# Kernel optimization log

Measured on AMD Instinct MI355X. Metric: run time of the kernel, lower is better.

The kernel has to match this reference:

```python
import jax, jax.numpy as jnp
import numpy as np

N_NODES = 50000
N_EDGES = 1600000
D = 128  # in_dim = hidden = out_dim = 128


def _gat_layer(x, W, b, aW, ab, src, dst, n_nodes):
    # fc: z = x @ W^T + b   (torch Linear convention, W:[out,in])
    z = x @ W.T + b                      # [N, d]
    d = z.shape[1]
    # attn_fc(concat(z_src, z_dst)) decomposed into per-node halves
    a_src = z @ aW[0, :d]                # [N]
    a_dst = z @ aW[0, d:]                # [N]
    e = jax.nn.leaky_relu(a_src[src] + a_dst[dst] + ab[0])  # [E], slope 0.01 (torch default)
    # segment softmax over incoming edges of each dst node
    m = jax.ops.segment_max(e, dst, num_segments=n_nodes)   # [N]
    ex = jnp.exp(e - m[dst])             # [E]
    s = jax.ops.segment_sum(ex, dst, num_segments=n_nodes)  # [N]
    alpha = ex / s[dst]                  # [E]
    # weighted scatter-sum of source features
    h = jax.ops.segment_sum(alpha[:, None] * z[src], dst, num_segments=n_nodes)  # [N, d]
    return h


def setup_inputs() -> dict:
    key = jax.random.key(0)
    ks = jax.random.split(key, 16)
    x = jax.random.normal(ks[0], (N_NODES, D), dtype=jnp.float32)
    src = jax.random.randint(ks[1], (N_EDGES,), 0, N_NODES, dtype=jnp.int32)
    dst = jax.random.randint(ks[2], (N_EDGES,), 0, N_NODES, dtype=jnp.int32)
    inp = {"x": x, "src": src, "dst": dst, "t": 0}
    # 3 GAT layers (128->128, 128->128, 128->128); xavier-ish scale
    for i in range(3):
        base = 3 + 4 * i
        inp[f"W{i}"] = jax.random.normal(ks[base], (D, D), dtype=jnp.float32) * (1.0 / np.sqrt(D))
        inp[f"b{i}"] = jnp.zeros((D,), dtype=jnp.float32)
        inp[f"aW{i}"] = jax.random.normal(ks[base + 1], (1, 2 * D), dtype=jnp.float32) * (1.0 / np.sqrt(2 * D))
        inp[f"ab{i}"] = jnp.zeros((1,), dtype=jnp.float32)
    return inp


def reference(x, src, dst, t, W0, b0, aW0, ab0, W1, b1, aW1, ab1, W2, b2, aW2, ab2):
    n = x.shape[0]
    h = _gat_layer(x, W0, b0, aW0, ab0, src, dst, n)
    h = jax.nn.relu(h)
    h = _gat_layer(h, W1, b1, aW1, ab1, src, dst, n)
    h = jax.nn.relu(h)
    h = _gat_layer(h, W2, b2, aW2, ab2, src, dst, n)
    return h
```

## Files before the change

### kernel.cpp

```cpp
#include <hip/hip_runtime.h>
#include <hip/hip_fp16.h>
#include <math.h>

#define DD 128
#define NBKT 391
#define P1CHUNK 4096
#define P2CAP 8192


__global__ __launch_bounds__(256) void fill_zero_i(int* p, int n) {
    int i = blockIdx.x * 256 + threadIdx.x;
    if (i < n) p[i] = 0;
}


__global__ __launch_bounds__(512) void p1hist_k(const int* __restrict__ dst, int* __restrict__ gcount, int E) {
    __shared__ int lh[NBKT];
    const int tid = threadIdx.x;
    for (int i = tid; i < NBKT; i += 512) lh[i] = 0;
    __syncthreads();
    const int blk0 = blockIdx.x * P1CHUNK;
    const int blkE = min(blk0 + P1CHUNK, E);
    int i0 = blk0 + tid * 8;
    if (i0 + 8 <= blkE) {
        int4 d0 = *reinterpret_cast<const int4*>(dst + i0);
        int4 d1 = *reinterpret_cast<const int4*>(dst + i0 + 4);
        atomicAdd(&lh[d0.x >> 7], 1); atomicAdd(&lh[d0.y >> 7], 1);
        atomicAdd(&lh[d0.z >> 7], 1); atomicAdd(&lh[d0.w >> 7], 1);
        atomicAdd(&lh[d1.x >> 7], 1); atomicAdd(&lh[d1.y >> 7], 1);
        atomicAdd(&lh[d1.z >> 7], 1); atomicAdd(&lh[d1.w >> 7], 1);
    } else {
        for (int j = 0; j < 8; ++j) {
            int i = i0 + j;
            if (i < blkE) atomicAdd(&lh[dst[i] >> 7], 1);
        }
    }
    __syncthreads();
    for (int i = tid; i < NBKT; i += 512)
        if (lh[i]) atomicAdd(&gcount[i], lh[i]);
}


__global__ __launch_bounds__(512) void p1scan_k(const int* __restrict__ gcount, int* __restrict__ bbase,
                                                int* __restrict__ bcur, int E) {
    __shared__ int tmp[512];
    int t = threadIdx.x;
    int v = (t < NBKT) ? gcount[t] : 0;
    tmp[t] = v;
    __syncthreads();
#pragma unroll
    for (int o = 1; o < 512; o <<= 1) {
        int add = (t >= o) ? tmp[t - o] : 0;
        __syncthreads();
        tmp[t] += add;
        __syncthreads();
    }
    if (t <= NBKT) {
        int ex = (t < NBKT) ? (tmp[t] - v) : E;
        bbase[t] = ex;
        if (t < NBKT) bcur[t] = ex;
    }
}


__global__ __launch_bounds__(512) void p1scatter_k(const int* __restrict__ src, const int* __restrict__ dst,
                                                   int* __restrict__ bcur, int2* __restrict__ bufA, int E) {
    __shared__ int lcnt[NBKT];
    __shared__ int lstart[512];
    __shared__ int blkb[NBKT];
    __shared__ int2 stage[P1CHUNK];
    const int tid = threadIdx.x;
    for (int i = tid; i < NBKT; i += 512) lcnt[i] = 0;
    __syncthreads();
    const int blk0 = blockIdx.x * P1CHUNK;
    const int blkE = min(blk0 + P1CHUNK, E);
    const int i0 = blk0 + tid * 8;

    int sv[8], dv[8], bn[8], rk[8], cntT = 0;
    if (i0 + 8 <= blkE) {
        int4 s0 = *reinterpret_cast<const int4*>(src + i0);
        int4 s1 = *reinterpret_cast<const int4*>(src + i0 + 4);
        int4 d0 = *reinterpret_cast<const int4*>(dst + i0);
        int4 d1 = *reinterpret_cast<const int4*>(dst + i0 + 4);
        sv[0] = s0.x; sv[1] = s0.y; sv[2] = s0.z; sv[3] = s0.w;
        sv[4] = s1.x; sv[5] = s1.y; sv[6] = s1.z; sv[7] = s1.w;
        dv[0] = d0.x; dv[1] = d0.y; dv[2] = d0.z; dv[3] = d0.w;
        dv[4] = d1.x; dv[5] = d1.y; dv[6] = d1.z; dv[7] = d1.w;
        cntT = 8;
    } else {
#pragma unroll
        for (int j = 0; j < 8; ++j) {
            int i = i0 + j;
            if (i < blkE) { sv[j] = src[i]; dv[j] = dst[i]; cntT = j + 1; }
        }
    }
#pragma unroll
    for (int j = 0; j < 8; ++j) {
        if (j < cntT) {
            bn[j] = dv[j] >> 7;
            rk[j] = atomicAdd(&lcnt[bn[j]], 1);
        }
    }
    __syncthreads();
    int v = (tid < NBKT) ? lcnt[tid] : 0;
    lstart[tid] = v;
    __syncthreads();
#pragma unroll
    for (int o = 1; o < 512; o <<= 1) {
        int add = (tid >= o) ? lstart[tid - o] : 0;
        __syncthreads();
        lstart[tid] += add;
        __syncthreads();
    }
    lstart[tid] -= v;
    __syncthreads();
    for (int i = tid; i < NBKT; i += 512)
        blkb[i] = lcnt[i] ? atomicAdd(&bcur[i], lcnt[i]) : 0;
#pragma unroll
    for (int j = 0; j < 8; ++j) {
        if (j < cntT) {
            int pos = lstart[bn[j]] + rk[j];
            stage[pos] = make_int2(sv[j], dv[j]);
        }
    }
    __syncthreads();
    const int cnt = blkE - blk0;
    for (int j = tid; j < cnt; j += 512) {
        int2 e = stage[j];
        int b = e.y >> 7;
        bufA[blkb[b] + (j - lstart[b])] = e;
    }
}


__global__ __launch_bounds__(512) void p2sort_k(const int2* __restrict__ bufA, const int* __restrict__ bbase,
                                                int* __restrict__ srcs, int* __restrict__ dstS) {
    __shared__ int h2[128];
    __shared__ int start2[128];
    __shared__ int cur2[128];
    __shared__ int ssrc[P2CAP];
    __shared__ int sdst[P2CAP];
    const int tid = threadIdx.x;
    const int b = blockIdx.x;
    const int base = bbase[b];
    const int cnt = bbase[b + 1] - base;
    for (int i = tid; i < 128; i += 512) h2[i] = 0;
    __syncthreads();
    for (int j = tid; j < cnt; j += 512)
        atomicAdd(&h2[bufA[base + j].y & 127], 1);
    __syncthreads();
    if (tid == 0) {
        int s = 0;
        for (int i = 0; i < 128; ++i) { start2[i] = s; cur2[i] = s; s += h2[i]; }
    }
    __syncthreads();
    for (int j = tid; j < cnt; j += 512) {
        int2 e = bufA[base + j];
        int p = atomicAdd(&cur2[e.y & 127], 1);
        ssrc[p] = e.x;
        sdst[p] = e.y;
    }
    __syncthreads();
    for (int j = tid; j < cnt; j += 512) {
        srcs[base + j] = ssrc[j];
        dstS[base + j] = sdst[j];
    }
}


__global__ __launch_bounds__(512) void off_k(const int* __restrict__ dstS, int* __restrict__ off, int N, int E) {
    int i = blockIdx.x * 512 + threadIdx.x;
    if (i >= E) return;
    int d = dstS[i];
    int p = (i == 0) ? -1 : dstS[i - 1];
    if (d != p)
        for (int n = p + 1; n <= d; ++n) off[n] = i;
    if (i == E - 1)
        for (int n = d + 1; n <= N; ++n) off[n] = E;
}


__global__ __launch_bounds__(256) void gemm_k(const float* __restrict__ X, const float* __restrict__ W,
                                              const float* __restrict__ B, const float* __restrict__ aW,
                                              __half* __restrict__ Zh, float* __restrict__ a_src,
                                              float* __restrict__ a_dst, int N) {
    __shared__ __align__(16) float xs[32][64];
    __shared__ __align__(16) float ws[32][128];
    const int tid = threadIdx.x;
    const int row0 = blockIdx.x * 64;
    const int cg = tid & 31;
    const int rg = tid >> 5;
    float acc[8][4];
#pragma unroll
    for (int i = 0; i < 8; ++i)
#pragma unroll
        for (int j = 0; j < 4; ++j) acc[i][j] = 0.f;

    for (int kc = 0; kc < DD; kc += 32) {
        {
            int r = tid >> 2;
            int k4 = (tid & 3) * 8;
            int gr = row0 + r;
            if (gr >= N) gr = N - 1;
            const float4* p = reinterpret_cast<const float4*>(X + (size_t)gr * DD + kc + k4);
            float4 v0 = p[0], v1 = p[1];
            xs[k4 + 0][r] = v0.x; xs[k4 + 1][r] = v0.y; xs[k4 + 2][r] = v0.z; xs[k4 + 3][r] = v0.w;
            xs[k4 + 4][r] = v1.x; xs[k4 + 5][r] = v1.y; xs[k4 + 6][r] = v1.z; xs[k4 + 7][r] = v1.w;
        }
        {
            int o = tid >> 1;
            int k8 = (tid & 1) * 16;
            const float4* p = reinterpret_cast<const float4*>(W + (size_t)o * DD + kc + k8);
            float4 v0 = p[0], v1 = p[1], v2 = p[2], v3 = p[3];
            ws[k8 + 0][o] = v0.x;  ws[k8 + 1][o] = v0.y;  ws[k8 + 2][o] = v0.z;  ws[k8 + 3][o] = v0.w;
            ws[k8 + 4][o] = v1.x;  ws[k8 + 5][o] = v1.y;  ws[k8 + 6][o] = v1.z;  ws[k8 + 7][o] = v1.w;
            ws[k8 + 8][o] = v2.x;  ws[k8 + 9][o] = v2.y;  ws[k8 + 10][o] = v2.z; ws[k8 + 11][o] = v2.w;
            ws[k8 + 12][o] = v3.x; ws[k8 + 13][o] = v3.y; ws[k8 + 14][o] = v3.z; ws[k8 + 15][o] = v3.w;
        }
        __syncthreads();
#pragma unroll
        for (int k = 0; k < 32; ++k) {
            const float4 wv = *reinterpret_cast<const float4*>(&ws[k][cg * 4]);
            const float4 xa = *reinterpret_cast<const float4*>(&xs[k][rg * 8]);
            const float4 xb = *reinterpret_cast<const float4*>(&xs[k][rg * 8 + 4]);
            float xr[8] = {xa.x, xa.y, xa.z, xa.w, xb.x, xb.y, xb.z, xb.w};
            float wr[4] = {wv.x, wv.y, wv.z, wv.w};
#pragma unroll
            for (int i = 0; i < 8; ++i)
#pragma unroll
                for (int j = 0; j < 4; ++j)
                    acc[i][j] = fmaf(xr[i], wr[j], acc[i][j]);
        }
        __syncthreads();
    }
    const int c0 = cg * 4;
    const float4 bv = *reinterpret_cast<const float4*>(B + c0);
    const float4 aw0 = *reinterpret_cast<const float4*>(aW + c0);
    const float4 aw1 = *reinterpret_cast<const float4*>(aW + DD + c0);
    float pa[8], pb[8];
#pragma unroll
    for (int i = 0; i < 8; ++i) {
        acc[i][0] += bv.x; acc[i][1] += bv.y; acc[i][2] += bv.z; acc[i][3] += bv.w;
        pa[i] = acc[i][0] * aw0.x + acc[i][1] * aw0.y + acc[i][2] * aw0.z + acc[i][3] * aw0.w;
        pb[i] = acc[i][0] * aw1.x + acc[i][1] * aw1.y + acc[i][2] * aw1.z + acc[i][3] * aw1.w;
    }
#pragma unroll
    for (int o = 1; o < 32; o <<= 1) {
#pragma unroll
        for (int i = 0; i < 8; ++i) {
            pa[i] += __shfl_xor(pa[i], o);
            pb[i] += __shfl_xor(pb[i], o);
        }
    }
    const int sl = c0 >> 5;
    const int cin = c0 & 31;
#pragma unroll
    for (int i = 0; i < 8; ++i) {
        int gr = row0 + rg * 8 + i;
        if (gr < N) {
            __half2 p0 = __floats2half2_rn(acc[i][0], acc[i][1]);
            __half2 p1 = __floats2half2_rn(acc[i][2], acc[i][3]);
            __half2* dst2 = reinterpret_cast<__half2*>(Zh + ((size_t)sl * N + gr) * 32 + cin);
            dst2[0] = p0;
            dst2[1] = p1;
            if (cg == 0) {
                a_src[gr] = pa[i];
                a_dst[gr] = pb[i];
            }
        }
    }
}


__global__ __launch_bounds__(256) void alpha_k(const float* __restrict__ a_src, const float* __restrict__ a_dst,
                                               const int* __restrict__ off, const int* __restrict__ srcs,
                                               const float* __restrict__ ab, int2* __restrict__ pair, int N) {
    int node = blockIdx.x * 4 + (threadIdx.x >> 6);
    int lane = threadIdx.x & 63;
    if (node >= N) return;
    const int beg = off[node], end = off[node + 1];
    const float adn = a_dst[node] + ab[0];
    const int i0 = beg + lane;
    float psum = 0.f;
    int s0 = 0; float p0 = 0.f;
    for (int i = i0; i < end; i += 64) {
        int s = srcs[i];
        float e = a_src[s] + adn;
        e = (e > 0.f) ? e : 0.01f * e;
        float p = __expf(e);
        if (i == i0) { s0 = s; p0 = p; }
        else pair[i] = make_int2(s, __float_as_int(p));
        psum += p;
    }
#pragma unroll
    for (int o = 1; o < 64; o <<= 1) psum += __shfl_xor(psum, o);
    const float inv = (end > beg) ? 1.0f / psum : 0.0f;
    if (i0 < end) pair[i0] = make_int2(s0, __float_as_int(p0 * inv));
    for (int i = i0 + 64; i < end; i += 64) {
        int2 pr = pair[i];
        pair[i] = make_int2(pr.x, __float_as_int(__int_as_float(pr.y) * inv));
    }
}


__global__ __launch_bounds__(256) void aggr_k(const __half* __restrict__ Zh, const int2* __restrict__ pair,
                                              const int* __restrict__ off, float* __restrict__ H,
                                              int N, int do_relu) {
    const int slice = blockIdx.x & 3;
    const int lane = threadIdx.x & 63;
    const int wid = threadIdx.x >> 6;
    const int ng = lane >> 5;
    const int node = (blockIdx.x >> 2) * 8 + wid * 2 + ng;
    if (node >= N) return;
    const int eg = (lane >> 2) & 7;
    const int ql = lane & 3;
    const int beg = off[node], end = off[node + 1];
    const __half* Zs = Zh + (size_t)slice * N * 32 + ql * 8;
    const long long* gp = reinterpret_cast<const long long*>(pair);

    float acc[8];
#pragma unroll
    for (int k = 0; k < 8; ++k) acc[k] = 0.f;

    for (int i = beg + eg; i < end; i += 16) {
        int i1 = i + 8;
        bool v1 = (i1 < end);
        long long pk0 = gp[i];
        long long pk1 = gp[v1 ? i1 : i];
        int s0 = (int)(pk0 & 0xffffffffll);
        int s1 = (int)(pk1 & 0xffffffffll);
        float a0 = __int_as_float((int)(pk0 >> 32));
        float a1 = v1 ? __int_as_float((int)(pk1 >> 32)) : 0.f;
        int4 r0 = *reinterpret_cast<const int4*>(Zs + (size_t)s0 * 32);
        int4 r1 = *reinterpret_cast<const int4*>(Zs + (size_t)s1 * 32);
        {
            float2 f0 = __half22float2(*reinterpret_cast<__half2*>(&r0.x));
            float2 f1 = __half22float2(*reinterpret_cast<__half2*>(&r0.y));
            float2 f2 = __half22float2(*reinterpret_cast<__half2*>(&r0.z));
            float2 f3 = __half22float2(*reinterpret_cast<__half2*>(&r0.w));
            acc[0] = fmaf(a0, f0.x, acc[0]); acc[1] = fmaf(a0, f0.y, acc[1]);
            acc[2] = fmaf(a0, f1.x, acc[2]); acc[3] = fmaf(a0, f1.y, acc[3]);
            acc[4] = fmaf(a0, f2.x, acc[4]); acc[5] = fmaf(a0, f2.y, acc[5]);
            acc[6] = fmaf(a0, f3.x, acc[6]); acc[7] = fmaf(a0, f3.y, acc[7]);
        }
        {
            float2 f0 = __half22float2(*reinterpret_cast<__half2*>(&r1.x));
            float2 f1 = __half22float2(*reinterpret_cast<__half2*>(&r1.y));
            float2 f2 = __half22float2(*reinterpret_cast<__half2*>(&r1.z));
            float2 f3 = __half22float2(*reinterpret_cast<__half2*>(&r1.w));
            acc[0] = fmaf(a1, f0.x, acc[0]); acc[1] = fmaf(a1, f0.y, acc[1]);
            acc[2] = fmaf(a1, f1.x, acc[2]); acc[3] = fmaf(a1, f1.y, acc[3]);
            acc[4] = fmaf(a1, f2.x, acc[4]); acc[5] = fmaf(a1, f2.y, acc[5]);
            acc[6] = fmaf(a1, f3.x, acc[6]); acc[7] = fmaf(a1, f3.y, acc[7]);
        }
    }
#pragma unroll
    for (int o = 4; o <= 16; o <<= 1) {
#pragma unroll
        for (int k = 0; k < 8; ++k) acc[k] += __shfl_xor(acc[k], o);
    }
    if (eg == 0) {
#pragma unroll
        for (int k = 0; k < 8; ++k)
            if (do_relu) acc[k] = fmaxf(acc[k], 0.f);
        float* out = H + (size_t)node * DD + slice * 32 + ql * 8;
#pragma unroll
        for (int k = 0; k < 8; ++k)
            __builtin_nontemporal_store(acc[k], out + k);
    }
}


extern "C" void kernel_launch(void* const* d_in, const int* in_sizes, int n_in,
                              void* d_out, int out_size, void* d_ws, size_t ws_size,
                              hipStream_t stream) {
    const float* x  = (const float*)d_in[0];
    const int* src  = (const int*)d_in[1];
    const int* dst  = (const int*)d_in[2];
    const float* Wl[3]  = {(const float*)d_in[4],  (const float*)d_in[8],  (const float*)d_in[12]};
    const float* bl[3]  = {(const float*)d_in[5],  (const float*)d_in[9],  (const float*)d_in[13]};
    const float* aWl[3] = {(const float*)d_in[6],  (const float*)d_in[10], (const float*)d_in[14]};
    const float* abl[3] = {(const float*)d_in[7],  (const float*)d_in[11], (const float*)d_in[15]};
    const int N = in_sizes[0] / DD;
    const int E = in_sizes[1];

    char* p = (char*)d_ws;
    auto alloc = [&](size_t bytes) -> char* {
        char* r = p;
        p += (bytes + 255) & ~(size_t)255;
        return r;
    };
    __half* zh  = (__half*)alloc((size_t)N * DD * 2);
    float* hA   = (float*)alloc((size_t)N * DD * 4);
    float* hB   = (float*)alloc((size_t)N * DD * 4);
    float* asrc = (float*)alloc((size_t)N * 4);
    float* adst = (float*)alloc((size_t)N * 4);
    int* off    = (int*)alloc((size_t)(N + 1) * 4);
    int* srcs   = (int*)alloc((size_t)E * 4);
    int2* pair  = (int2*)alloc((size_t)E * 8);
    int* gcount = (int*)alloc(512 * 4);
    int* bbase  = (int*)alloc(512 * 4);
    int* bcur   = (int*)alloc(512 * 4);
    int2* bufA  = (int2*)hB;
    int* dstS   = (int*)hA;

    const int NBLK1 = (E + P1CHUNK - 1) / P1CHUNK;

    fill_zero_i<<<2, 256, 0, stream>>>(gcount, 512);
    p1hist_k<<<NBLK1, 512, 0, stream>>>(dst, gcount, E);
    p1scan_k<<<1, 512, 0, stream>>>(gcount, bbase, bcur, E);
    p1scatter_k<<<NBLK1, 512, 0, stream>>>(src, dst, bcur, bufA, E);
    p2sort_k<<<NBKT, 512, 0, stream>>>(bufA, bbase, srcs, dstS);
    off_k<<<(E + 511) / 512, 512, 0, stream>>>(dstS, off, N, E);

    const float* in = x;
    float* outs[3] = {hA, hB, (float*)d_out};
    const int node_blocks = (N + 3) / 4;
    const int aggr_blocks = 4 * ((N + 7) / 8);
    for (int l = 0; l < 3; ++l) {
        gemm_k<<<(N + 63) / 64, 256, 0, stream>>>(in, Wl[l], bl[l], aWl[l], zh, asrc, adst, N);
        alpha_k<<<node_blocks, 256, 0, stream>>>(asrc, adst, off, srcs, abl[l], pair, N);
        aggr_k<<<aggr_blocks, 256, 0, stream>>>(zh, pair, off, outs[l], N, (l < 2) ? 1 : 0);
        in = outs[l];
    }
}
```

Before: 340.2 us.

## Pack edge source and fp16 alpha into 32-bit words; enlarge GEMM tile

```diff
diff --git a/kernel.cpp b/kernel.cpp
--- a/kernel.cpp
+++ b/kernel.cpp
@@ -180,14 +180,14 @@
 }
 
 
-__global__ __launch_bounds__(256) void gemm_k(const float* __restrict__ X, const float* __restrict__ W,
+__global__ __launch_bounds__(512) void gemm_k(const float* __restrict__ X, const float* __restrict__ W,
                                               const float* __restrict__ B, const float* __restrict__ aW,
                                               __half* __restrict__ Zh, float* __restrict__ a_src,
                                               float* __restrict__ a_dst, int N) {
-    __shared__ __align__(16) float xs[32][64];
+    __shared__ __align__(16) float xs[32][128];
     __shared__ __align__(16) float ws[32][128];
     const int tid = threadIdx.x;
-    const int row0 = blockIdx.x * 64;
+    const int row0 = blockIdx.x * 128;
     const int cg = tid & 31;
     const int rg = tid >> 5;
     float acc[8][4];
@@ -208,14 +208,12 @@
             xs[k4 + 4][r] = v1.x; xs[k4 + 5][r] = v1.y; xs[k4 + 6][r] = v1.z; xs[k4 + 7][r] = v1.w;
         }
         {
-            int o = tid >> 1;
-            int k8 = (tid & 1) * 16;
+            int o = tid >> 2;
+            int k8 = (tid & 3) * 8;
             const float4* p = reinterpret_cast<const float4*>(W + (size_t)o * DD + kc + k8);
-            float4 v0 = p[0], v1 = p[1], v2 = p[2], v3 = p[3];
-            ws[k8 + 0][o] = v0.x;  ws[k8 + 1][o] = v0.y;  ws[k8 + 2][o] = v0.z;  ws[k8 + 3][o] = v0.w;
-            ws[k8 + 4][o] = v1.x;  ws[k8 + 5][o] = v1.y;  ws[k8 + 6][o] = v1.z;  ws[k8 + 7][o] = v1.w;
-            ws[k8 + 8][o] = v2.x;  ws[k8 + 9][o] = v2.y;  ws[k8 + 10][o] = v2.z; ws[k8 + 11][o] = v2.w;
-            ws[k8 + 12][o] = v3.x; ws[k8 + 13][o] = v3.y; ws[k8 + 14][o] = v3.z; ws[k8 + 15][o] = v3.w;
+            float4 v0 = p[0], v1 = p[1];
+            ws[k8 + 0][o] = v0.x; ws[k8 + 1][o] = v0.y; ws[k8 + 2][o] = v0.z; ws[k8 + 3][o] = v0.w;
+            ws[k8 + 4][o] = v1.x; ws[k8 + 5][o] = v1.y; ws[k8 + 6][o] = v1.z; ws[k8 + 7][o] = v1.w;
         }
         __syncthreads();
 #pragma unroll
@@ -274,36 +272,52 @@
 
 __global__ __launch_bounds__(256) void alpha_k(const float* __restrict__ a_src, const float* __restrict__ a_dst,
                                                const int* __restrict__ off, const int* __restrict__ srcs,
-                                               const float* __restrict__ ab, int2* __restrict__ pair, int N) {
+                                               const float* __restrict__ ab, unsigned* __restrict__ pairc, int N) {
     int node = blockIdx.x * 4 + (threadIdx.x >> 6);
     int lane = threadIdx.x & 63;
     if (node >= N) return;
     const int beg = off[node], end = off[node + 1];
+    const int deg = end - beg;
     const float adn = a_dst[node] + ab[0];
-    const int i0 = beg + lane;
-    float psum = 0.f;
-    int s0 = 0; float p0 = 0.f;
-    for (int i = i0; i < end; i += 64) {
-        int s = srcs[i];
-        float e = a_src[s] + adn;
-        e = (e > 0.f) ? e : 0.01f * e;
-        float p = __expf(e);
-        if (i == i0) { s0 = s; p0 = p; }
-        else pair[i] = make_int2(s, __float_as_int(p));
-        psum += p;
-    }
-#pragma unroll
-    for (int o = 1; o < 64; o <<= 1) psum += __shfl_xor(psum, o);
-    const float inv = (end > beg) ? 1.0f / psum : 0.0f;
-    if (i0 < end) pair[i0] = make_int2(s0, __float_as_int(p0 * inv));
-    for (int i = i0 + 64; i < end; i += 64) {
-        int2 pr = pair[i];
-        pair[i] = make_int2(pr.x, __float_as_int(__int_as_float(pr.y) * inv));
-    }
-}
-
-
-__global__ __launch_bounds__(256) void aggr_k(const __half* __restrict__ Zh, const int2* __restrict__ pair,
+    if (deg <= 64) {
+        int i = beg + lane;
+        float p = 0.f; int s = 0;
+        if (i < end) {
+            s = srcs[i];
+            float e = a_src[s] + adn;
+            e = (e > 0.f) ? e : 0.01f * e;
+            p = __expf(e);
+        }
+        float psum = p;
+#pragma unroll
+        for (int o = 1; o < 64; o <<= 1) psum += __shfl_xor(psum, o);
+        float inv = (deg > 0) ? 1.0f / psum : 0.0f;
+        if (i < end) {
+            unsigned ah = __half_as_ushort(__float2half(p * inv));
+            pairc[i] = (ah << 16) | (unsigned)s;
+        }
+    } else {
+        float psum = 0.f;
+        for (int i = beg + lane; i < end; i += 64) {
+            float e = a_src[srcs[i]] + adn;
+            e = (e > 0.f) ? e : 0.01f * e;
+            psum += __expf(e);
+        }
+#pragma unroll
+        for (int o = 1; o < 64; o <<= 1) psum += __shfl_xor(psum, o);
+        const float inv = 1.0f / psum;
+        for (int i = beg + lane; i < end; i += 64) {
+            int s = srcs[i];
+            float e = a_src[s] + adn;
+            e = (e > 0.f) ? e : 0.01f * e;
+            unsigned ah = __half_as_ushort(__float2half(__expf(e) * inv));
+            pairc[i] = (ah << 16) | (unsigned)s;
+        }
+    }
+}
+
+
+__global__ __launch_bounds__(256) void aggr_k(const __half* __restrict__ Zh, const unsigned* __restrict__ pairc,
                                               const int* __restrict__ off, float* __restrict__ H,
                                               int N, int do_relu) {
     const int slice = blockIdx.x & 3;
@@ -316,43 +330,36 @@
     const int ql = lane & 3;
     const int beg = off[node], end = off[node + 1];
     const __half* Zs = Zh + (size_t)slice * N * 32 + ql * 8;
-    const long long* gp = reinterpret_cast<const long long*>(pair);
 
     float acc[8];
 #pragma unroll
     for (int k = 0; k < 8; ++k) acc[k] = 0.f;
 
-    for (int i = beg + eg; i < end; i += 16) {
-        int i1 = i + 8;
-        bool v1 = (i1 < end);
-        long long pk0 = gp[i];
-        long long pk1 = gp[v1 ? i1 : i];
-        int s0 = (int)(pk0 & 0xffffffffll);
-        int s1 = (int)(pk1 & 0xffffffffll);
-        float a0 = __int_as_float((int)(pk0 >> 32));
-        float a1 = v1 ? __int_as_float((int)(pk1 >> 32)) : 0.f;
+    int i = beg + eg;
+    for (; i + 8 < end; i += 16) {
+        unsigned w0 = pairc[i];
+        unsigned w1 = pairc[i + 8];
+        int s0 = (int)(w0 & 0xffffu);
+        int s1 = (int)(w1 & 0xffffu);
+        float a0 = __half2float(__ushort_as_half((unsigned short)(w0 >> 16)));
+        float a1 = __half2float(__ushort_as_half((unsigned short)(w1 >> 16)));
         int4 r0 = *reinterpret_cast<const int4*>(Zs + (size_t)s0 * 32);
         int4 r1 = *reinterpret_cast<const int4*>(Zs + (size_t)s1 * 32);
-        {
-            float2 f0 = __half22float2(*reinterpret_cast<__half2*>(&r0.x));
-            float2 f1 = __half22float2(*reinterpret_cast<__half2*>(&r0.y));
-            float2 f2 = __half22float2(*reinterpret_cast<__half2*>(&r0.z));
-            float2 f3 = __half22float2(*reinterpret_cast<__half2*>(&r0.w));
-            acc[0] = fmaf(a0, f0.x, acc[0]); acc[1] = fmaf(a0, f0.y, acc[1]);
-            acc[2] = fmaf(a0, f1.x, acc[2]); acc[3] = fmaf(a0, f1.y, acc[3]);
-            acc[4] = fmaf(a0, f2.x, acc[4]); acc[5] = fmaf(a0, f2.y, acc[5]);
-            acc[6] = fmaf(a0, f3.x, acc[6]); acc[7] = fmaf(a0, f3.y, acc[7]);
-        }
-        {
-            float2 f0 = __half22float2(*reinterpret_cast<__half2*>(&r1.x));
-            float2 f1 = __half22float2(*reinterpret_cast<__half2*>(&r1.y));
-            float2 f2 = __half22float2(*reinterpret_cast<__half2*>(&r1.z));
-            float2 f3 = __half22float2(*reinterpret_cast<__half2*>(&r1.w));
-            acc[0] = fmaf(a1, f0.x, acc[0]); acc[1] = fmaf(a1, f0.y, acc[1]);
-            acc[2] = fmaf(a1, f1.x, acc[2]); acc[3] = fmaf(a1, f1.y, acc[3]);
-            acc[4] = fmaf(a1, f2.x, acc[4]); acc[5] = fmaf(a1, f2.y, acc[5]);
-            acc[6] = fmaf(a1, f3.x, acc[6]); acc[7] = fmaf(a1, f3.y, acc[7]);
-        }
+        const __half* h0 = reinterpret_cast<const __half*>(&r0);
+        const __half* h1 = reinterpret_cast<const __half*>(&r1);
+#pragma unroll
+        for (int k = 0; k < 8; ++k) acc[k] = fmaf(a0, __half2float(h0[k]), acc[k]);
+#pragma unroll
+        for (int k = 0; k < 8; ++k) acc[k] = fmaf(a1, __half2float(h1[k]), acc[k]);
+    }
+    if (i < end) {
+        unsigned w0 = pairc[i];
+        int s0 = (int)(w0 & 0xffffu);
+        float a0 = __half2float(__ushort_as_half((unsigned short)(w0 >> 16)));
+        int4 r0 = *reinterpret_cast<const int4*>(Zs + (size_t)s0 * 32);
+        const __half* h0 = reinterpret_cast<const __half*>(&r0);
+#pragma unroll
+        for (int k = 0; k < 8; ++k) acc[k] = fmaf(a0, __half2float(h0[k]), acc[k]);
     }
 #pragma unroll
     for (int o = 4; o <= 16; o <<= 1) {
@@ -397,7 +404,7 @@
     float* adst = (float*)alloc((size_t)N * 4);
     int* off    = (int*)alloc((size_t)(N + 1) * 4);
     int* srcs   = (int*)alloc((size_t)E * 4);
-    int2* pair  = (int2*)alloc((size_t)E * 8);
+    unsigned* pairc = (unsigned*)alloc((size_t)E * 4);
     int* gcount = (int*)alloc(512 * 4);
     int* bbase  = (int*)alloc(512 * 4);
     int* bcur   = (int*)alloc(512 * 4);
@@ -418,9 +425,9 @@
     const int node_blocks = (N + 3) / 4;
     const int aggr_blocks = 4 * ((N + 7) / 8);
     for (int l = 0; l < 3; ++l) {
-        gemm_k<<<(N + 63) / 64, 256, 0, stream>>>(in, Wl[l], bl[l], aWl[l], zh, asrc, adst, N);
-        alpha_k<<<node_blocks, 256, 0, stream>>>(asrc, adst, off, srcs, abl[l], pair, N);
-        aggr_k<<<aggr_blocks, 256, 0, stream>>>(zh, pair, off, outs[l], N, (l < 2) ? 1 : 0);
+        gemm_k<<<(N + 127) / 128, 512, 0, stream>>>(in, Wl[l], bl[l], aWl[l], zh, asrc, adst, N);
+        alpha_k<<<node_blocks, 256, 0, stream>>>(asrc, adst, off, srcs, abl[l], pairc, N);
+        aggr_k<<<aggr_blocks, 256, 0, stream>>>(zh, pairc, off, outs[l], N, (l < 2) ? 1 : 0);
         in = outs[l];
     }
 }
```

Measured after the change: 325.5 us. 1.05x faster.
